# Kernel tuning notes

Hardware: AMD Instinct MI355X
Metric: run time of the kernel (lower is better)

## Reference

```python
import jax, jax.numpy as jnp
import numpy as np

# --- module hyperparameters (from init_kwargs) ---
NUM_HEADS = 16
ATTN_DIM = 1024
HEAD_DIM = ATTN_DIM // NUM_HEADS  # 64
NUM_RF = 256                      # FAVOR random features per head
CONV_CH = 1024
GROUPS = 4
M_SCALE = 256                     # num_features_per_scale
GAMMAS = (0.5, 1.0, 2.0)          # gamma_list
NY_LANDMARKS = 64                 # == HEAD_DIM so shapes compose
NY_GAMMA = 1.0
EPS = 1e-6


def setup_inputs() -> dict:
    key = jax.random.key(0)
    ks = jax.random.split(key, 12)
    B, S, C = 2, 4096, CONV_CH
    G, Ms = len(GAMMAS), M_SCALE
    x = jax.random.normal(ks[0], (B, S, C), dtype=jnp.float32)
    # grouped Conv1D kernels (WIO layout): [ksize, Cin/groups, Cout], one per q/k/v
    conv_k = jax.random.normal(ks[1], (3, 3, C // GROUPS, C), jnp.float32) / np.sqrt(3 * (C // GROUPS))
    conv_b = jnp.zeros((3, C), jnp.float32)
    # multi-scale random-Fourier-feature weights per projection and per gamma scale
    rff_w = jax.random.normal(ks[2], (3, G, C, Ms), jnp.float32)
    rff_b = jax.random.uniform(ks[3], (3, G, Ms), jnp.float32) * (2.0 * np.pi)
    proj_w = jax.random.normal(ks[4], (3, G * Ms, ATTN_DIM), jnp.float32) / np.sqrt(G * Ms)
    proj_b = jnp.zeros((3, ATTN_DIM), jnp.float32)
    # FAVOR+ projection matrix (shared across heads) and Nystrom landmarks
    omega = jax.random.normal(ks[5], (HEAD_DIM, NUM_RF), jnp.float32)
    landmarks = jax.random.normal(ks[6], (NY_LANDMARKS, HEAD_DIM), jnp.float32)
    out_w = jax.random.normal(ks[7], (ATTN_DIM, ATTN_DIM), jnp.float32) / np.sqrt(ATTN_DIM)
    out_b = jnp.zeros((ATTN_DIM,), jnp.float32)
    return {"x": x, "conv_k": conv_k, "conv_b": conv_b, "rff_w": rff_w, "rff_b": rff_b,
            "proj_w": proj_w, "proj_b": proj_b, "omega": omega, "landmarks": landmarks,
            "out_w": out_w, "out_b": out_b}


def _rotary(seq_len, dh, dtype):
    inv = 1.0 / (10000.0 ** (jnp.arange(0, dh, 2, dtype=jnp.float32) / dh))
    f = jnp.arange(seq_len, dtype=jnp.float32)[:, None] * inv[None, :]  # [S, dh/2]
    emb = jnp.concatenate([f, f], axis=-1)  # [S, dh]
    return jnp.sin(emb).astype(dtype), jnp.cos(emb).astype(dtype)


def _apply_rope(x, sin, cos):
    # x: [B,H,S,D]; rotate-half RoPE
    d = x.shape[-1] // 2
    rot = jnp.concatenate([-x[..., d:], x[..., :d]], axis=-1)
    return x * cos + rot * sin


def _projection(x, ck, cb, rw, rb, pw, pb):
    # ProjectionWithKernel: grouped conv -> multi-scale RFF kernel map -> dense
    h = jax.lax.conv_general_dilated(x, ck, (1,), 'SAME',
                                     dimension_numbers=('NWC', 'WIO', 'NWC'),
                                     feature_group_count=GROUPS) + cb
    g = jnp.sqrt(2.0 * jnp.array(GAMMAS, dtype=x.dtype))[:, None]  # [G,1]
    z = jnp.cos(jnp.einsum('bsc,gcm->bsgm', h, rw) * g + rb)       # [B,S,G,Ms]
    feats = (z * jnp.sqrt(2.0 / M_SCALE)).reshape(x.shape[0], x.shape[1], -1)
    return feats @ pw + pb  # [B,S,ATTN_DIM]


def _favor(x, omega):
    # FAVOR+ positive random features: exp(x.w - |x|^2/2) / sqrt(m)
    norm = 0.5 * jnp.sum(x * x, axis=-1, keepdims=True)
    return jnp.exp(jnp.einsum('bhsd,dm->bhsm', x, omega) - norm) / jnp.sqrt(float(omega.shape[-1]))


def _nystrom(k, landmarks):
    # RBF features against landmarks (normalized by dim to keep exp in range)
    d = k.shape[-1]
    d2 = (jnp.sum(k * k, -1, keepdims=True) + jnp.sum(landmarks * landmarks, -1)
          - 2.0 * jnp.einsum('bhsd,ld->bhsl', k, landmarks))
    return jnp.exp(-NY_GAMMA * d2 / d)  # [B,H,S,L], L == HEAD_DIM


def reference(x, conv_k, conv_b, rff_w, rff_b, proj_w, proj_b, omega, landmarks, out_w, out_b):
    B, S, _ = x.shape
    qkv = [_projection(x, conv_k[i], conv_b[i], rff_w[i], rff_b[i], proj_w[i], proj_b[i])
           for i in range(3)]
    split = lambda t: t.reshape(B, S, NUM_HEADS, HEAD_DIM).transpose(0, 2, 1, 3)
    q, k, v = map(split, qkv)  # [B,H,S,Dh]
    sin, cos = _rotary(S, HEAD_DIM, x.dtype)
    q = _apply_rope(q, sin, cos)
    k = _apply_rope(k, sin, cos)
    k = _nystrom(k, landmarks)               # [B,H,S,Dh]
    qp = _favor(q, omega)                    # [B,H,S,M]
    kp = _favor(k, omega)                    # [B,H,S,M]
    denom = jnp.einsum('bhse,bhe->bhs', qp, jnp.sum(kp, axis=2))[..., None]
    kv = jnp.einsum('bhse,bhsd->bhed', kp, v)          # [B,H,M,Dh]
    num = jnp.einsum('bhse,bhed->bhsd', qp, kv)        # [B,H,S,Dh]
    out = num / (denom + EPS)
    out = out.transpose(0, 2, 1, 3).reshape(B, S, ATTN_DIM)
    return out @ out_w + out_b  # dropout is identity at inference
```

## Files before the change

### kernel.cpp

```cpp
#include <hip/hip_runtime.h>
#include <math.h>


using f32x4 = __attribute__((ext_vector_type(4))) float;
using s16x8 = __attribute__((ext_vector_type(8))) short;

__device__ __forceinline__ unsigned short f2bf(float x) {
  unsigned u = __float_as_uint(x);
  unsigned r = u + 0x7fffu + ((u >> 16) & 1u);
  return (unsigned short)(r >> 16);
}
__device__ __forceinline__ float bf2f(unsigned short h) {
  return __uint_as_float(((unsigned)h) << 16);
}

__device__ __forceinline__ void gload16(const void* g, void* l) {
  __builtin_amdgcn_global_load_lds(
      (const __attribute__((address_space(1))) void*)g,
      (__attribute__((address_space(3))) void*)l, 16, 0, 0);
}

__global__ __launch_bounds__(256) void split_prep_kernel(
    const float* __restrict__ in, unsigned short* __restrict__ ohi,
    unsigned short* __restrict__ olo, int n8)
{
  const int i = blockIdx.x * 256 + threadIdx.x;
  if (i >= n8) return;
  const float4 f0 = ((const float4*)in)[i * 2];
  const float4 f1 = ((const float4*)in)[i * 2 + 1];
  const float v[8] = {f0.x, f0.y, f0.z, f0.w, f1.x, f1.y, f1.z, f1.w};
  s16x8 hi, lo;
  #pragma unroll
  for (int u = 0; u < 8; ++u) {
    const unsigned short hh = f2bf(v[u]);
    hi[u] = (short)hh;
    lo[u] = (short)f2bf(v[u] - bf2f(hh));
  }
  ((s16x8*)ohi)[i] = hi;
  ((s16x8*)olo)[i] = lo;
}

template<int WM>
__global__ __launch_bounds__(256) void wconv_kernel(
    const float* __restrict__ in0, unsigned short* __restrict__ ohi,
    unsigned short* __restrict__ olo)
{
  int K, N;
  const float* in;
  unsigned short *oh, *ol = nullptr;
  const int z = blockIdx.z;
  if constexpr (WM == 0) {
    K = 768; N = 1024;
    in = in0 + (size_t)z * 786432;
    oh = ohi + (size_t)z * 786432; ol = olo + (size_t)z * 786432;
  } else if constexpr (WM == 1) {
    K = 1024; N = 256;
    const int i = z / 3, g = z % 3;
    in = in0 + (size_t)i * 786432 + (size_t)g * 262144;
    oh = ohi + (size_t)i * 786432 + (size_t)g * 262144;
    ol = olo + (size_t)i * 786432 + (size_t)g * 262144;
  } else if constexpr (WM == 2) {
    K = 768; N = 1024;
    in = in0 + (size_t)z * 786432; oh = ohi + (size_t)z * 786432;
  } else {
    K = 1024; N = 1024; in = in0; oh = ohi;
  }
  const int k0 = blockIdx.x * 64, n0 = blockIdx.y * 64;
  __shared__ float t[64][65];
  const int tid = threadIdx.x, tn = tid & 63, tr = tid >> 6;
  #pragma unroll 4
  for (int p = 0; p < 16; ++p) {
    const int kk = p * 4 + tr;
    t[kk][tn] = in[(size_t)(k0 + kk) * N + n0 + tn];
  }
  __syncthreads();
  #pragma unroll 4
  for (int p = 0; p < 16; ++p) {
    const int nn = p * 4 + tr;
    const float v = t[tn][nn];
    const unsigned short hi = f2bf(v);
    oh[(size_t)(n0 + nn) * K + k0 + tn] = hi;
    if constexpr (WM <= 1)
      ol[(size_t)(n0 + nn) * K + k0 + tn] = f2bf(v - bf2f(hi));
  }
}

__global__ __launch_bounds__(256) void omega_prep_kernel(
    const float* __restrict__ omega, unsigned short* __restrict__ oThi,
    unsigned short* __restrict__ oTlo)
{
  const int idx = blockIdx.x * 256 + threadIdx.x;
  const int m = idx >> 6, d = idx & 63;
  const float v = omega[d * 256 + m];
  const unsigned short hi = f2bf(v);
  oThi[idx] = hi;
  oTlo[idx] = f2bf(v - bf2f(hi));
}

__global__ __launch_bounds__(256) void vt_kernel(
    const float* __restrict__ V, unsigned short* __restrict__ VT)
{
  const int bh = blockIdx.x, sb = blockIdx.y;
  const int b = bh >> 4, h = bh & 15;
  __shared__ float t[64][65];
  const int tid = threadIdx.x, tn = tid & 63, tr = tid >> 6;
  #pragma unroll 4
  for (int p = 0; p < 16; ++p)
    t[p * 4 + tr][tn] =
        V[(size_t)(b * 4096 + sb * 64 + p * 4 + tr) * 1024 + h * 64 + tn];
  __syncthreads();
  #pragma unroll 4
  for (int p = 0; p < 16; ++p)
    VT[((size_t)bh * 80 + p * 4 + tr) * 4096 + sb * 64 + tn] =
        f2bf(t[tn][p * 4 + tr]);
  #pragma unroll
  for (int p = 0; p < 4; ++p) {
    const int rr = p * 4 + tr;
    VT[((size_t)bh * 80 + 64 + rr) * 4096 + sb * 64 + tn] =
        (rr == 0) ? 0x3F80 : 0;
  }
}

template<int MODE>
__global__ __launch_bounds__(256, MODE >= 2 ? 4 : 3) void gemm_mfma(
    const unsigned short* __restrict__ Ahi, const unsigned short* __restrict__ Alo,
    const unsigned short* __restrict__ Bhig, const unsigned short* __restrict__ Blog,
    const float* __restrict__ bias, const float2* __restrict__ tab,
    float* __restrict__ Cf, unsigned short* __restrict__ C1,
    unsigned short* __restrict__ C2,
    int M, int N, int K)
{
  constexpr bool SPLIT = (MODE <= 1);
  __shared__ alignas(16) char smem[SPLIT ? 32768 : 16384];
  char* const sAhi = smem;
  char* const sBhi = smem + (SPLIT ? 16384 : 8192);
  char* const sAlo = smem + 8192;
  char* const sBlo = smem + 24576;

  const int gx = gridDim.x, gy = gridDim.y;
  const int L = blockIdx.x + gx * (blockIdx.y + gy * blockIdx.z);
  const int nwg = gx * gy * gridDim.z;
  const int logical = (L & 7) * (nwg >> 3) + (L >> 3);
  const int bx = logical % gx;
  const int by = (logical / gx) % gy;
  const int z = logical / (gx * gy);

  if constexpr (MODE == 0) {
    Bhig += (size_t)z * 786432; Blog += (size_t)z * 786432;
    bias += z * 1024;
    C1 += (size_t)z * 8388608; C2 += (size_t)z * 8388608;
  } else if constexpr (MODE == 1) {
    Ahi += (size_t)z * 8388608; Alo += (size_t)z * 8388608;
    Bhig += (size_t)z * 786432; Blog += (size_t)z * 786432;
    bias += z * 768;
    C1 += (size_t)z * 6291456;
  } else if constexpr (MODE == 2) {
    Ahi += (size_t)z * 6291456;
    Bhig += (size_t)z * 786432;
    bias += z * 1024;
    Cf += (size_t)z * 8388608;
  }

  const int tid = threadIdx.x;
  const int n0 = bx * 128;
  const int m0 = by * 128;

  const int lane = tid & 63, wid = tid >> 6;
  const int wr = wid >> 1, wc = wid & 1;
  const int fr = lane & 15, kc = lane >> 4;
  const int fsw = ((fr >> 1) & 3) << 4;

  const int seg0 = wid * 2;
  const int r0 = seg0 * 16 + (lane >> 2);
  const int r1 = r0 + 16;
  const int cp = lane & 3;
  const int c0e = (cp ^ ((r0 >> 1) & 3)) * 8;
  const int c1e = (cp ^ ((r1 >> 1) & 3)) * 8;
  char* const dA0 = sAhi + seg0 * 1024;  char* const dA1 = dA0 + 1024;
  char* const dL0 = sAlo + seg0 * 1024;  char* const dL1 = dL0 + 1024;
  char* const dB0 = sBhi + seg0 * 1024;  char* const dB1 = dB0 + 1024;
  char* const dBl0 = sBlo + seg0 * 1024; char* const dBl1 = dBl0 + 1024;

  f32x4 acc[4][4];
  #pragma unroll
  for (int i = 0; i < 4; ++i)
    #pragma unroll
    for (int j = 0; j < 4; ++j) acc[i][j] = f32x4{0.f, 0.f, 0.f, 0.f};

  for (int k0 = 0; k0 < K; k0 += 32) {
    __syncthreads();
    if constexpr (MODE == 0) {
      const int t = k0 >> 8;
      const int cb = (n0 >> 8) * 256 + (k0 & 255);
      const int g0 = m0 + r0, g1 = m0 + r1;
      int s0 = (g0 & 4095) + t - 1; s0 = s0 < 0 ? 0 : (s0 > 4095 ? 4095 : s0);
      int s1 = (g1 & 4095) + t - 1; s1 = s1 < 0 ? 0 : (s1 > 4095 ? 4095 : s1);
      const size_t o0 = ((size_t)((g0 >> 12) * 4096 + s0)) * 1024 + cb;
      const size_t o1 = ((size_t)((g1 >> 12) * 4096 + s1)) * 1024 + cb;
      gload16(Ahi + o0 + c0e, dA0);
      gload16(Ahi + o1 + c1e, dA1);
      gload16(Alo + o0 + c0e, dL0);
      gload16(Alo + o1 + c1e, dL1);
    } else {
      const size_t o0 = (size_t)(m0 + r0) * K + k0;
      const size_t o1 = (size_t)(m0 + r1) * K + k0;
      gload16(Ahi + o0 + c0e, dA0);
      gload16(Ahi + o1 + c1e, dA1);
      if constexpr (SPLIT) {
        gload16(Alo + o0 + c0e, dL0);
        gload16(Alo + o1 + c1e, dL1);
      }
    }
    {
      const size_t o0 = (size_t)(n0 + r0) * K + k0;
      const size_t o1 = (size_t)(n0 + r1) * K + k0;
      gload16(Bhig + o0 + c0e, dB0);
      gload16(Bhig + o1 + c1e, dB1);
      if constexpr (SPLIT) {
        gload16(Blog + o0 + c0e, dBl0);
        gload16(Blog + o1 + c1e, dBl1);
      }
    }
    __syncthreads();

    if constexpr (MODE == 0) {
      const int t = k0 >> 8;
      int zr = -1;
      if (t == 0 && (m0 & 4095) == 0) zr = 0;
      if (t == 2 && (m0 & 4095) == 3968) zr = 127;
      if (zr >= 0) {
        if (tid < 8) {
          char* buf = (tid < 4) ? sAhi : sAlo;
          *(s16x8*)(buf + zr * 64 + (tid & 3) * 16) = s16x8{0,0,0,0,0,0,0,0};
        }
        __syncthreads();
      }
    }

    s16x8 Af[4], Al[4], Bf[4], Bl[4];
    #pragma unroll
    for (int i = 0; i < 4; ++i) {
      const int off = (wr * 64 + i * 16 + fr) * 64 + ((kc * 16) ^ fsw);
      Af[i] = *(const s16x8*)(sAhi + off);
      if constexpr (SPLIT) Al[i] = *(const s16x8*)(sAlo + off);
    }
    #pragma unroll
    for (int j = 0; j < 4; ++j) {
      const int off = (wc * 64 + j * 16 + fr) * 64 + ((kc * 16) ^ fsw);
      Bf[j] = *(const s16x8*)(sBhi + off);
      if constexpr (SPLIT) Bl[j] = *(const s16x8*)(sBlo + off);
    }
    #pragma unroll
    for (int i = 0; i < 4; ++i)
      #pragma unroll
      for (int j = 0; j < 4; ++j) {
        acc[i][j] = __builtin_amdgcn_mfma_f32_16x16x32_bf16(Af[i], Bf[j], acc[i][j], 0, 0, 0);
        if constexpr (SPLIT) {
          acc[i][j] = __builtin_amdgcn_mfma_f32_16x16x32_bf16(Af[i], Bl[j], acc[i][j], 0, 0, 0);
          acc[i][j] = __builtin_amdgcn_mfma_f32_16x16x32_bf16(Al[i], Bf[j], acc[i][j], 0, 0, 0);
        }
      }
  }

  if constexpr (MODE == 2) {
    #pragma unroll
    for (int i = 0; i < 4; ++i)
      #pragma unroll
      for (int j2 = 0; j2 < 2; ++j2) {
        const int col0 = n0 + wc * 64 + j2 * 16 + fr;
        const int jr = col0 & 31;
        const float b0 = bias[col0], b1 = bias[col0 + 32];
        #pragma unroll
        for (int rr = 0; rr < 4; ++rr) {
          const int row = m0 + wr * 64 + i * 16 + kc * 4 + rr;
          float v0 = acc[i][j2][rr] + b0;
          float v1 = acc[i][j2 + 2][rr] + b1;
          if (z < 2) {
            const float2 cs = tab[((row & 4095) << 5) | jr];
            const float rr0 = v0 * cs.x - v1 * cs.y;
            const float rr1 = v1 * cs.x + v0 * cs.y;
            v0 = rr0; v1 = rr1;
          }
          Cf[(size_t)row * N + col0] = v0;
          Cf[(size_t)row * N + col0 + 32] = v1;
        }
      }
  } else {
    #pragma unroll
    for (int i = 0; i < 4; ++i)
      #pragma unroll
      for (int j = 0; j < 4; ++j) {
        const int col = n0 + wc * 64 + j * 16 + fr;
        #pragma unroll
        for (int rr = 0; rr < 4; ++rr) {
          const int row = m0 + wr * 64 + i * 16 + kc * 4 + rr;
          const float v = acc[i][j][rr];
          if constexpr (MODE == 0) {
            const float hv = v + bias[col];
            const unsigned short hh = f2bf(hv);
            C1[(size_t)row * N + col] = hh;
            C2[(size_t)row * N + col] = f2bf(hv - bf2f(hh));
          } else if constexpr (MODE == 1) {
            const int g = col >> 8;
            const float sg = (g == 0) ? 1.0f : ((g == 1) ? 1.41421356237309515f : 2.0f);
            const float zc = cosf(v * sg + bias[col]) * 0.08838834764831845f;
            C1[(size_t)row * N + col] = f2bf(zc);
          } else {
            Cf[(size_t)row * N + col] = v + bias[col];
          }
        }
      }
  }
}

__global__ __launch_bounds__(256) void rope_table_kernel(float2* __restrict__ tab)
{
  const int idx = blockIdx.x * 256 + threadIdx.x;
  const int j = idx & 31, s = idx >> 5;
  const double inv = pow(10000.0, -(double)j * (1.0 / 32.0));
  double sd, cd;
  sincos((double)s * inv, &sd, &cd);
  tab[idx] = make_float2((float)cd, (float)sd);
}

__global__ __launch_bounds__(256) void nystrom_kernel(
    const float* __restrict__ Kb, const float* __restrict__ lm,
    float* __restrict__ kny)
{
  __shared__ float lmT[64][65];
  __shared__ float lnorm[64];
  const int tid = threadIdx.x;
  for (int idx = tid; idx < 4096; idx += 256)
    lmT[idx & 63][idx >> 6] = lm[idx];
  if (tid < 64) {
    float s = 0.f;
    #pragma unroll
    for (int d = 0; d < 64; ++d) { const float v = lm[tid * 64 + d]; s = fmaf(v, v, s); }
    lnorm[tid] = s;
  }
  __syncthreads();
  const int lane = tid & 63;
  const int nw = gridDim.x * 4;
  for (int row = blockIdx.x * 4 + (tid >> 6); row < 131072; row += nw) {
    const float kd = Kb[(size_t)row * 64 + lane];
    float nk = kd * kd;
    #pragma unroll
    for (int o = 32; o > 0; o >>= 1) nk += __shfl_xor(nk, o, 64);
    float dot = 0.f;
    #pragma unroll
    for (int d = 0; d < 64; ++d) dot = fmaf(__shfl(kd, d, 64), lmT[d][lane], dot);
    kny[(size_t)row * 64 + lane] = __expf((2.f * dot - nk - lnorm[lane]) * 0.015625f);
  }
}

__global__ __launch_bounds__(512) void favor_k_mfma(
    const float* __restrict__ kny,
    const unsigned short* __restrict__ oThi, const unsigned short* __restrict__ oTlo,
    const unsigned short* __restrict__ VT, float* __restrict__ KVp)
{
  const int bid = blockIdx.x;
  const int bh = bid >> 3, chunk = bid & 7;
  const int b = bh >> 4, h = bh & 15;
  const int s0 = chunk * 512;
  const int tid = threadIdx.x, lane = tid & 63, wid = tid >> 6;
  const int fr = lane & 15, kc = lane >> 4;
  const int m0w = wid * 32;

  __shared__ unsigned short P[256][40];
  __shared__ float T[8][32][84];

  s16x8 whi[2][2], wlo[2][2];
  #pragma unroll
  for (int c = 0; c < 2; ++c)
    #pragma unroll
    for (int ks = 0; ks < 2; ++ks) {
      const size_t off = (size_t)(m0w + c * 16 + fr) * 64 + ks * 32 + kc * 8;
      whi[c][ks] = *(const s16x8*)(oThi + off);
      wlo[c][ks] = *(const s16x8*)(oTlo + off);
    }

  f32x4 acc2[2][5];
  #pragma unroll
  for (int i = 0; i < 2; ++i)
    #pragma unroll
    for (int j = 0; j < 5; ++j) acc2[i][j] = f32x4{0.f, 0.f, 0.f, 0.f};

  for (int st = 0; st < 512; st += 32) {
    s16x8 ahi[2][2], alo[2][2];
    float nrm[2];
    #pragma unroll
    for (int r = 0; r < 2; ++r) {
      float part = 0.f;
      #pragma unroll
      for (int ks = 0; ks < 2; ++ks) {
        const float* ap = kny +
            ((size_t)((b * 4096 + s0 + st + r * 16 + fr) * 16 + h)) * 64 + ks * 32 + kc * 8;
        const float4 f0 = ((const float4*)ap)[0];
        const float4 f1 = ((const float4*)ap)[1];
        float v[8] = {f0.x, f0.y, f0.z, f0.w, f1.x, f1.y, f1.z, f1.w};
        #pragma unroll
        for (int u = 0; u < 8; ++u) {
          part = fmaf(v[u], v[u], part);
          const unsigned short hh = f2bf(v[u]);
          ahi[r][ks][u] = (short)hh;
          alo[r][ks][u] = (short)f2bf(v[u] - bf2f(hh));
        }
      }
      part += __shfl_xor(part, 16);
      part += __shfl_xor(part, 32);
      nrm[r] = 0.5f * part;
    }
    __syncthreads();
    #pragma unroll
    for (int r = 0; r < 2; ++r)
      #pragma unroll
      for (int c = 0; c < 2; ++c) {
        f32x4 s1 = f32x4{0.f, 0.f, 0.f, 0.f};
        #pragma unroll
        for (int ks = 0; ks < 2; ++ks) {
          s1 = __builtin_amdgcn_mfma_f32_16x16x32_bf16(alo[r][ks], whi[c][ks], s1, 0, 0, 0);
          s1 = __builtin_amdgcn_mfma_f32_16x16x32_bf16(ahi[r][ks], wlo[c][ks], s1, 0, 0, 0);
          s1 = __builtin_amdgcn_mfma_f32_16x16x32_bf16(ahi[r][ks], whi[c][ks], s1, 0, 0, 0);
        }
        #pragma unroll
        for (int reg = 0; reg < 4; ++reg) {
          const int sl = kc * 4 + reg;
          const float nn = __shfl(nrm[r], sl);
          const float p = __expf(s1[reg] - nn - 2.772588722239781f);
          P[m0w + c * 16 + fr][r * 16 + sl] = f2bf(p);
        }
      }
    __syncthreads();
    s16x8 b2[5];
    #pragma unroll
    for (int nf = 0; nf < 5; ++nf)
      b2[nf] = *(const s16x8*)(VT + ((size_t)bh * 80 + nf * 16 + fr) * 4096 +
                               s0 + st + kc * 8);
    #pragma unroll
    for (int mf = 0; mf < 2; ++mf) {
      const s16x8 a2 = *(const s16x8*)&P[m0w + mf * 16 + fr][kc * 8];
      #pragma unroll
      for (int nf = 0; nf < 5; ++nf)
        acc2[mf][nf] = __builtin_amdgcn_mfma_f32_16x16x32_bf16(a2, b2[nf], acc2[mf][nf], 0, 0, 0);
    }
  }
  #pragma unroll
  for (int mf = 0; mf < 2; ++mf)
    #pragma unroll
    for (int nf = 0; nf < 5; ++nf)
      #pragma unroll
      for (int reg = 0; reg < 4; ++reg)
        T[wid][mf * 16 + kc * 4 + reg][nf * 16 + fr] = acc2[mf][nf][reg];
  __syncthreads();
  #pragma unroll
  for (int i = 0; i < 40; ++i) {
    const int flat = i * 64 + lane;
    const int n = flat >> 5, ml = flat & 31;
    KVp[((size_t)bid * 80 + n) * 256 + m0w + ml] = T[wid][ml][n];
  }
}

__global__ __launch_bounds__(256) void reduce_kvxt_kernel(
    const float* __restrict__ KVp, unsigned short* __restrict__ KVXT)
{
  const int bh = blockIdx.x;
  const int m = threadIdx.x;
  for (int n = 0; n < 80; ++n) {
    float s = 0.f;
    #pragma unroll
    for (int c = 0; c < 8; ++c)
      s += KVp[((size_t)(bh * 8 + c) * 80 + n) * 256 + m];
    KVXT[((size_t)bh * 80 + n) * 256 + m] = f2bf(s);
  }
}

__global__ __launch_bounds__(512) void favor_q_mfma(
    const float* __restrict__ Q,
    const unsigned short* __restrict__ oThi, const unsigned short* __restrict__ oTlo,
    const unsigned short* __restrict__ KVXT, unsigned short* __restrict__ O)
{
  const int bid = blockIdx.x;
  const int bh = bid >> 4, chunk = bid & 15;
  const int b = bh >> 4, h = bh & 15;
  const int s0 = chunk * 256;
  const int tid = threadIdx.x, lane = tid & 63, wid = tid >> 6;
  const int fr = lane & 15, kc = lane >> 4;
  const int ws0 = s0 + wid * 32;

  __shared__ unsigned short KX[80][264];
  __shared__ unsigned short P[8][32][66];

  for (int i = tid; i < 80 * 256; i += 512)
    KX[i >> 8][i & 255] = KVXT[(size_t)bh * 80 * 256 + i];
  __syncthreads();

  s16x8 ahi[2][2], alo[2][2];
  float nrm[2];
  #pragma unroll
  for (int r = 0; r < 2; ++r) {
    float part = 0.f;
    #pragma unroll
    for (int ks = 0; ks < 2; ++ks) {
      const float* ap = Q + ((size_t)(b * 4096 + ws0 + r * 16 + fr)) * 1024 +
                        h * 64 + ks * 32 + kc * 8;
      const float4 f0 = ((const float4*)ap)[0];
      const float4 f1 = ((const float4*)ap)[1];
      float v[8] = {f0.x, f0.y, f0.z, f0.w, f1.x, f1.y, f1.z, f1.w};
      #pragma unroll
      for (int u = 0; u < 8; ++u) {
        part = fmaf(v[u], v[u], part);
        const unsigned short hh = f2bf(v[u]);
        ahi[r][ks][u] = (short)hh;
        alo[r][ks][u] = (short)f2bf(v[u] - bf2f(hh));
      }
    }
    part += __shfl_xor(part, 16);
    part += __shfl_xor(part, 32);
    nrm[r] = 0.5f * part;
  }

  f32x4 acc2[2][5];
  #pragma unroll
  for (int i = 0; i < 2; ++i)
    #pragma unroll
    for (int j = 0; j < 5; ++j) acc2[i][j] = f32x4{0.f, 0.f, 0.f, 0.f};

  for (int mc = 0; mc < 4; ++mc) {
    __syncthreads();
    #pragma unroll
    for (int r = 0; r < 2; ++r)
      #pragma unroll
      for (int c = 0; c < 4; ++c) {
        f32x4 s1 = f32x4{0.f, 0.f, 0.f, 0.f};
        #pragma unroll
        for (int ks = 0; ks < 2; ++ks) {
          const size_t off = (size_t)(mc * 64 + c * 16 + fr) * 64 + ks * 32 + kc * 8;
          const s16x8 bh1 = *(const s16x8*)(oThi + off);
          const s16x8 bl1 = *(const s16x8*)(oTlo + off);
          s1 = __builtin_amdgcn_mfma_f32_16x16x32_bf16(alo[r][ks], bh1, s1, 0, 0, 0);
          s1 = __builtin_amdgcn_mfma_f32_16x16x32_bf16(ahi[r][ks], bl1, s1, 0, 0, 0);
          s1 = __builtin_amdgcn_mfma_f32_16x16x32_bf16(ahi[r][ks], bh1, s1, 0, 0, 0);
        }
        #pragma unroll
        for (int reg = 0; reg < 4; ++reg) {
          const int sl = kc * 4 + reg;
          const float nn = __shfl(nrm[r], sl);
          const float p = __expf(s1[reg] - nn - 2.772588722239781f);
          P[wid][r * 16 + sl][c * 16 + fr] = f2bf(p);
        }
      }
    __syncthreads();
    #pragma unroll
    for (int ks2 = 0; ks2 < 2; ++ks2) {
      s16x8 b2[5];
      #pragma unroll
      for (int nf = 0; nf < 5; ++nf)
        b2[nf] = *(const s16x8*)&KX[nf * 16 + fr][mc * 64 + ks2 * 32 + kc * 8];
      #pragma unroll
      for (int r = 0; r < 2; ++r) {
        const s16x8 a2 = *(const s16x8*)&P[wid][r * 16 + fr][ks2 * 32 + kc * 8];
        #pragma unroll
        for (int nf = 0; nf < 5; ++nf)
          acc2[r][nf] = __builtin_amdgcn_mfma_f32_16x16x32_bf16(a2, b2[nf], acc2[r][nf], 0, 0, 0);
      }
    }
  }
  #pragma unroll
  for (int r = 0; r < 2; ++r)
    #pragma unroll
    for (int reg = 0; reg < 4; ++reg) {
      const int s = ws0 + r * 16 + kc * 4 + reg;
      const float dv = __shfl(acc2[r][4][reg], lane & 48) + 1e-6f;
      #pragma unroll
      for (int nf = 0; nf < 4; ++nf)
        O[(size_t)(b * 4096 + s) * 1024 + h * 64 + nf * 16 + fr] =
            f2bf(acc2[r][nf][reg] / dv);
    }
}

extern "C" void kernel_launch(void* const* d_in, const int* in_sizes, int n_in,
                              void* d_out, int out_size, void* d_ws, size_t ws_size,
                              hipStream_t stream)
{
  const float* x      = (const float*)d_in[0];
  const float* conv_k = (const float*)d_in[1];
  const float* conv_b = (const float*)d_in[2];
  const float* rff_w  = (const float*)d_in[3];
  const float* rff_b  = (const float*)d_in[4];
  const float* proj_w = (const float*)d_in[5];
  const float* proj_b = (const float*)d_in[6];
  const float* omega  = (const float*)d_in[7];
  const float* lm     = (const float*)d_in[8];
  const float* out_w  = (const float*)d_in[9];
  const float* out_b  = (const float*)d_in[10];

  char* wsb = (char*)d_ws;
  size_t o = 0;
  auto alloc = [&](size_t bytes) {
    char* p = wsb + o;
    o = (o + bytes + 255) & ~(size_t)255;
    return p;
  };
  unsigned short* Wc_hi = (unsigned short*)alloc(4718592);
  unsigned short* Wc_lo = (unsigned short*)alloc(4718592);
  unsigned short* Wr_hi = (unsigned short*)alloc(4718592);
  unsigned short* Wr_lo = (unsigned short*)alloc(4718592);
  unsigned short* Wp    = (unsigned short*)alloc(4718592);
  unsigned short* Wo    = (unsigned short*)alloc(2097152);
  unsigned short* oThi  = (unsigned short*)alloc(32768);
  unsigned short* oTlo  = (unsigned short*)alloc(32768);
  float2* tab           = (float2*)alloc(1048576);
  char* RB = alloc(41943040);
  unsigned short* xhi   = (unsigned short*)RB;
  unsigned short* xlo   = (unsigned short*)(RB + 16777216);
  unsigned short* feats = (unsigned short*)RB;
  unsigned short* VT    = (unsigned short*)RB;
  unsigned short* Obf   = (unsigned short*)(RB + 20971520);
  unsigned short* KVXT  = (unsigned short*)(RB + 37748736);
  char* RC = alloc(100663296);
  unsigned short* hhi   = (unsigned short*)RC;
  unsigned short* hlo   = (unsigned short*)(RC + 50331648);
  float* QKV            = (float*)RC;
  float* kny = (float*)alloc(33554432);
  float* KVp = (float*)alloc(20971520);

  dim3 blk(256);
  split_prep_kernel<<<4096, blk, 0, stream>>>(x, xhi, xlo, 1048576);
  wconv_kernel<0><<<dim3(12, 16, 3), blk, 0, stream>>>(conv_k, Wc_hi, Wc_lo);
  wconv_kernel<1><<<dim3(16, 4, 9),  blk, 0, stream>>>(rff_w, Wr_hi, Wr_lo);
  wconv_kernel<2><<<dim3(12, 16, 3), blk, 0, stream>>>(proj_w, Wp, nullptr);
  wconv_kernel<3><<<dim3(16, 16, 1), blk, 0, stream>>>(out_w, Wo, nullptr);
  omega_prep_kernel<<<64, blk, 0, stream>>>(omega, oThi, oTlo);
  rope_table_kernel<<<512, blk, 0, stream>>>(tab);

  gemm_mfma<0><<<dim3(8, 64, 3), blk, 0, stream>>>(
      xhi, xlo, Wc_hi, Wc_lo, conv_b, nullptr,
      nullptr, hhi, hlo, 8192, 1024, 768);
  gemm_mfma<1><<<dim3(6, 64, 3), blk, 0, stream>>>(
      hhi, hlo, Wr_hi, Wr_lo, rff_b, nullptr,
      nullptr, feats, nullptr, 8192, 768, 1024);
  gemm_mfma<2><<<dim3(8, 64, 3), blk, 0, stream>>>(
      feats, nullptr, Wp, nullptr, proj_b, tab,
      QKV, nullptr, nullptr, 8192, 1024, 768);

  float* Qb = QKV;
  float* Kb = QKV + 8388608;
  float* Vb = QKV + 16777216;
  vt_kernel<<<dim3(32, 64), blk, 0, stream>>>(Vb, VT);
  nystrom_kernel<<<512, blk, 0, stream>>>(Kb, lm, kny);
  favor_k_mfma<<<256, dim3(512), 0, stream>>>(kny, oThi, oTlo, VT, KVp);
  reduce_kvxt_kernel<<<32, blk, 0, stream>>>(KVp, KVXT);
  favor_q_mfma<<<512, dim3(512), 0, stream>>>(Qb, oThi, oTlo, KVXT, Obf);
  gemm_mfma<3><<<dim3(8, 64), blk, 0, stream>>>(
      Obf, nullptr, Wo, nullptr, out_b, nullptr,
      (float*)d_out, nullptr, nullptr, 8192, 1024, 1024);
}
```

Baseline: 1.058 ms.

## Drop bf16 hi/lo split in FAVOR stages and move Nystrom onto MFMA

Removes the three-term hi/lo bf16 emulation in favor_k and favor_q, using a single bf16 MFMA against bf16 omega. Rewrites the Nystrom kernel to use MFMA. It now writes bf16 kernel features plus precomputed half squared norms, which favor_k reads directly instead of recomputing. It also raises gemm_mfma launch bounds to 4 waves for the split modes. The aim is to cut MFMA count, memory traffic and conversion work, at the cost of lower precision in the feature maps and possibly more register pressure in the split GEMMs.

```diff
diff --git a/kernel.cpp b/kernel.cpp
--- a/kernel.cpp
+++ b/kernel.cpp
@@ -86,15 +86,11 @@
 }
 
 __global__ __launch_bounds__(256) void omega_prep_kernel(
-    const float* __restrict__ omega, unsigned short* __restrict__ oThi,
-    unsigned short* __restrict__ oTlo)
+    const float* __restrict__ omega, unsigned short* __restrict__ oThi)
 {
   const int idx = blockIdx.x * 256 + threadIdx.x;
   const int m = idx >> 6, d = idx & 63;
-  const float v = omega[d * 256 + m];
-  const unsigned short hi = f2bf(v);
-  oThi[idx] = hi;
-  oTlo[idx] = f2bf(v - bf2f(hi));
+  oThi[idx] = f2bf(omega[d * 256 + m]);
 }
 
 __global__ __launch_bounds__(256) void vt_kernel(
@@ -122,7 +118,7 @@
 }
 
 template<int MODE>
-__global__ __launch_bounds__(256, MODE >= 2 ? 4 : 3) void gemm_mfma(
+__global__ __launch_bounds__(256, 4) void gemm_mfma(
     const unsigned short* __restrict__ Ahi, const unsigned short* __restrict__ Alo,
     const unsigned short* __restrict__ Bhig, const unsigned short* __restrict__ Blog,
     const float* __restrict__ bias, const float2* __restrict__ tab,
@@ -323,15 +319,18 @@
   tab[idx] = make_float2((float)cd, (float)sd);
 }
 
-__global__ __launch_bounds__(256) void nystrom_kernel(
+__global__ __launch_bounds__(256) void nystrom_mfma(
     const float* __restrict__ Kb, const float* __restrict__ lm,
-    float* __restrict__ kny)
-{
-  __shared__ float lmT[64][65];
+    unsigned short* __restrict__ kny, float* __restrict__ knorm)
+{
+  const int bid = blockIdx.x;
+  const int bh = bid >> 4, chunk = bid & 15;
+  const int b = bh >> 4, h = bh & 15;
+  const int tid = threadIdx.x, lane = tid & 63, wid = tid >> 6;
+  const int fr = lane & 15, kc = lane >> 4;
+  const int ws0 = chunk * 256 + wid * 64;
+
   __shared__ float lnorm[64];
-  const int tid = threadIdx.x;
-  for (int idx = tid; idx < 4096; idx += 256)
-    lmT[idx & 63][idx >> 6] = lm[idx];
   if (tid < 64) {
     float s = 0.f;
     #pragma unroll
@@ -339,23 +338,69 @@
     lnorm[tid] = s;
   }
   __syncthreads();
-  const int lane = tid & 63;
-  const int nw = gridDim.x * 4;
-  for (int row = blockIdx.x * 4 + (tid >> 6); row < 131072; row += nw) {
-    const float kd = Kb[(size_t)row * 64 + lane];
-    float nk = kd * kd;
-    #pragma unroll
-    for (int o = 32; o > 0; o >>= 1) nk += __shfl_xor(nk, o, 64);
-    float dot = 0.f;
-    #pragma unroll
-    for (int d = 0; d < 64; ++d) dot = fmaf(__shfl(kd, d, 64), lmT[d][lane], dot);
-    kny[(size_t)row * 64 + lane] = __expf((2.f * dot - nk - lnorm[lane]) * 0.015625f);
+
+  s16x8 bfr[4][2];
+  #pragma unroll
+  for (int c = 0; c < 4; ++c)
+    #pragma unroll
+    for (int ks = 0; ks < 2; ++ks) {
+      const float* lp = lm + (c * 16 + fr) * 64 + ks * 32 + kc * 8;
+      #pragma unroll
+      for (int u = 0; u < 8; ++u) bfr[c][ks][u] = (short)f2bf(lp[u]);
+    }
+
+  #pragma unroll
+  for (int r = 0; r < 4; ++r) {
+    const int s_r = ws0 + r * 16 + fr;
+    const float* ap = Kb + ((size_t)(b * 4096 + s_r)) * 1024 + h * 64;
+    s16x8 afr[2];
+    float part = 0.f;
+    #pragma unroll
+    for (int ks = 0; ks < 2; ++ks) {
+      const float4 f0 = *(const float4*)(ap + ks * 32 + kc * 8);
+      const float4 f1 = *(const float4*)(ap + ks * 32 + kc * 8 + 4);
+      const float v[8] = {f0.x, f0.y, f0.z, f0.w, f1.x, f1.y, f1.z, f1.w};
+      #pragma unroll
+      for (int u = 0; u < 8; ++u) {
+        part = fmaf(v[u], v[u], part);
+        afr[ks][u] = (short)f2bf(v[u]);
+      }
+    }
+    part += __shfl_xor(part, 16);
+    part += __shfl_xor(part, 32);
+
+    float sq[4] = {0.f, 0.f, 0.f, 0.f};
+    #pragma unroll
+    for (int c = 0; c < 4; ++c) {
+      f32x4 acc = f32x4{0.f, 0.f, 0.f, 0.f};
+      acc = __builtin_amdgcn_mfma_f32_16x16x32_bf16(afr[0], bfr[c][0], acc, 0, 0, 0);
+      acc = __builtin_amdgcn_mfma_f32_16x16x32_bf16(afr[1], bfr[c][1], acc, 0, 0, 0);
+      const float ln = lnorm[c * 16 + fr];
+      #pragma unroll
+      for (int reg = 0; reg < 4; ++reg) {
+        const float nk = __shfl(part, kc * 4 + reg);
+        const float val = __expf((2.f * acc[reg] - nk - ln) * 0.015625f);
+        sq[reg] = fmaf(val, val, sq[reg]);
+        const int srow = ws0 + r * 16 + kc * 4 + reg;
+        kny[((size_t)(b * 4096 + srow) * 16 + h) * 64 + c * 16 + fr] = f2bf(val);
+      }
+    }
+    #pragma unroll
+    for (int reg = 0; reg < 4; ++reg) {
+      float s2 = sq[reg];
+      s2 += __shfl_xor(s2, 1); s2 += __shfl_xor(s2, 2);
+      s2 += __shfl_xor(s2, 4); s2 += __shfl_xor(s2, 8);
+      if (fr == 0) {
+        const int srow = ws0 + r * 16 + kc * 4 + reg;
+        knorm[(size_t)(b * 4096 + srow) * 16 + h] = 0.5f * s2;
+      }
+    }
   }
 }
 
 __global__ __launch_bounds__(512) void favor_k_mfma(
-    const float* __restrict__ kny,
-    const unsigned short* __restrict__ oThi, const unsigned short* __restrict__ oTlo,
+    const unsigned short* __restrict__ kny, const float* __restrict__ knorm,
+    const unsigned short* __restrict__ oThi,
     const unsigned short* __restrict__ VT, float* __restrict__ KVp)
 {
   const int bid = blockIdx.x;
@@ -369,15 +414,12 @@
   __shared__ unsigned short P[256][40];
   __shared__ float T[8][32][84];
 
-  s16x8 whi[2][2], wlo[2][2];
+  s16x8 whi[2][2];
   #pragma unroll
   for (int c = 0; c < 2; ++c)
     #pragma unroll
-    for (int ks = 0; ks < 2; ++ks) {
-      const size_t off = (size_t)(m0w + c * 16 + fr) * 64 + ks * 32 + kc * 8;
-      whi[c][ks] = *(const s16x8*)(oThi + off);
-      wlo[c][ks] = *(const s16x8*)(oTlo + off);
-    }
+    for (int ks = 0; ks < 2; ++ks)
+      whi[c][ks] = *(const s16x8*)(oThi + (size_t)(m0w + c * 16 + fr) * 64 + ks * 32 + kc * 8);
 
   f32x4 acc2[2][5];
   #pragma unroll
@@ -386,29 +428,14 @@
     for (int j = 0; j < 5; ++j) acc2[i][j] = f32x4{0.f, 0.f, 0.f, 0.f};
 
   for (int st = 0; st < 512; st += 32) {
-    s16x8 ahi[2][2], alo[2][2];
+    s16x8 a1[2][2];
     float nrm[2];
     #pragma unroll
     for (int r = 0; r < 2; ++r) {
-      float part = 0.f;
-      #pragma unroll
-      for (int ks = 0; ks < 2; ++ks) {
-        const float* ap = kny +
-            ((size_t)((b * 4096 + s0 + st + r * 16 + fr) * 16 + h)) * 64 + ks * 32 + kc * 8;
-        const float4 f0 = ((const float4*)ap)[0];
-        const float4 f1 = ((const float4*)ap)[1];
-        float v[8] = {f0.x, f0.y, f0.z, f0.w, f1.x, f1.y, f1.z, f1.w};
-        #pragma unroll
-        for (int u = 0; u < 8; ++u) {
-          part = fmaf(v[u], v[u], part);
-          const unsigned short hh = f2bf(v[u]);
-          ahi[r][ks][u] = (short)hh;
-          alo[r][ks][u] = (short)f2bf(v[u] - bf2f(hh));
-        }
-      }
-      part += __shfl_xor(part, 16);
-      part += __shfl_xor(part, 32);
-      nrm[r] = 0.5f * part;
+      const size_t kidx = (size_t)(b * 4096 + s0 + st + r * 16 + fr) * 16 + h;
+      a1[r][0] = *(const s16x8*)(kny + kidx * 64 + kc * 8);
+      a1[r][1] = *(const s16x8*)(kny + kidx * 64 + 32 + kc * 8);
+      nrm[r] = knorm[kidx];
     }
     __syncthreads();
     #pragma unroll
@@ -416,12 +443,8 @@
       #pragma unroll
       for (int c = 0; c < 2; ++c) {
         f32x4 s1 = f32x4{0.f, 0.f, 0.f, 0.f};
-        #pragma unroll
-        for (int ks = 0; ks < 2; ++ks) {
-          s1 = __builtin_amdgcn_mfma_f32_16x16x32_bf16(alo[r][ks], whi[c][ks], s1, 0, 0, 0);
-          s1 = __builtin_amdgcn_mfma_f32_16x16x32_bf16(ahi[r][ks], wlo[c][ks], s1, 0, 0, 0);
-          s1 = __builtin_amdgcn_mfma_f32_16x16x32_bf16(ahi[r][ks], whi[c][ks], s1, 0, 0, 0);
-        }
+        s1 = __builtin_amdgcn_mfma_f32_16x16x32_bf16(a1[r][0], whi[c][0], s1, 0, 0, 0);
+        s1 = __builtin_amdgcn_mfma_f32_16x16x32_bf16(a1[r][1], whi[c][1], s1, 0, 0, 0);
         #pragma unroll
         for (int reg = 0; reg < 4; ++reg) {
           const int sl = kc * 4 + reg;
@@ -475,8 +498,7 @@
 }
 
 __global__ __launch_bounds__(512) void favor_q_mfma(
-    const float* __restrict__ Q,
-    const unsigned short* __restrict__ oThi, const unsigned short* __restrict__ oTlo,
+    const float* __restrict__ Q, const unsigned short* __restrict__ oThi,
     const unsigned short* __restrict__ KVXT, unsigned short* __restrict__ O)
 {
   const int bid = blockIdx.x;
@@ -494,7 +516,7 @@
     KX[i >> 8][i & 255] = KVXT[(size_t)bh * 80 * 256 + i];
   __syncthreads();
 
-  s16x8 ahi[2][2], alo[2][2];
+  s16x8 ahi[2][2];
   float nrm[2];
   #pragma unroll
   for (int r = 0; r < 2; ++r) {
@@ -505,13 +527,11 @@
                         h * 64 + ks * 32 + kc * 8;
       const float4 f0 = ((const float4*)ap)[0];
       const float4 f1 = ((const float4*)ap)[1];
-      float v[8] = {f0.x, f0.y, f0.z, f0.w, f1.x, f1.y, f1.z, f1.w};
+      const float v[8] = {f0.x, f0.y, f0.z, f0.w, f1.x, f1.y, f1.z, f1.w};
       #pragma unroll
       for (int u = 0; u < 8; ++u) {
         part = fmaf(v[u], v[u], part);
-        const unsigned short hh = f2bf(v[u]);
-        ahi[r][ks][u] = (short)hh;
-        alo[r][ks][u] = (short)f2bf(v[u] - bf2f(hh));
+        ahi[r][ks][u] = (short)f2bf(v[u]);
       }
     }
     part += __shfl_xor(part, 16);
@@ -536,9 +556,6 @@
         for (int ks = 0; ks < 2; ++ks) {
           const size_t off = (size_t)(mc * 64 + c * 16 + fr) * 64 + ks * 32 + kc * 8;
           const s16x8 bh1 = *(const s16x8*)(oThi + off);
-          const s16x8 bl1 = *(const s16x8*)(oTlo + off);
-          s1 = __builtin_amdgcn_mfma_f32_16x16x32_bf16(alo[r][ks], bh1, s1, 0, 0, 0);
-          s1 = __builtin_amdgcn_mfma_f32_16x16x32_bf16(ahi[r][ks], bl1, s1, 0, 0, 0);
           s1 = __builtin_amdgcn_mfma_f32_16x16x32_bf16(ahi[r][ks], bh1, s1, 0, 0, 0);
         }
         #pragma unroll
@@ -621,8 +638,11 @@
   unsigned short* hhi   = (unsigned short*)RC;
   unsigned short* hlo   = (unsigned short*)(RC + 50331648);
   float* QKV            = (float*)RC;
-  float* kny = (float*)alloc(33554432);
+  char* RE = alloc(33554432);
+  unsigned short* knyb  = (unsigned short*)RE;
+  float* knorm          = (float*)(RE + 16777216);
   float* KVp = (float*)alloc(20971520);
+  (void)oTlo; (void)ws_size;
 
   dim3 blk(256);
   split_prep_kernel<<<4096, blk, 0, stream>>>(x, xhi, xlo, 1048576);
@@ -630,7 +650,7 @@
   wconv_kernel<1><<<dim3(16, 4, 9),  blk, 0, stream>>>(rff_w, Wr_hi, Wr_lo);
   wconv_kernel<2><<<dim3(12, 16, 3), blk, 0, stream>>>(proj_w, Wp, nullptr);
   wconv_kernel<3><<<dim3(16, 16, 1), blk, 0, stream>>>(out_w, Wo, nullptr);
-  omega_prep_kernel<<<64, blk, 0, stream>>>(omega, oThi, oTlo);
+  omega_prep_kernel<<<64, blk, 0, stream>>>(omega, oThi);
   rope_table_kernel<<<512, blk, 0, stream>>>(tab);
 
   gemm_mfma<0><<<dim3(8, 64, 3), blk, 0, stream>>>(
@@ -647,10 +667,10 @@
   float* Kb = QKV + 8388608;
   float* Vb = QKV + 16777216;
   vt_kernel<<<dim3(32, 64), blk, 0, stream>>>(Vb, VT);
-  nystrom_kernel<<<512, blk, 0, stream>>>(Kb, lm, kny);
-  favor_k_mfma<<<256, dim3(512), 0, stream>>>(kny, oThi, oTlo, VT, KVp);
+  nystrom_mfma<<<512, blk, 0, stream>>>(Kb, lm, knyb, knorm);
+  favor_k_mfma<<<256, dim3(512), 0, stream>>>(knyb, knorm, oThi, VT, KVp);
   reduce_kvxt_kernel<<<32, blk, 0, stream>>>(KVp, KVXT);
-  favor_q_mfma<<<512, dim3(512), 0, stream>>>(Qb, oThi, oTlo, KVXT, Obf);
+  favor_q_mfma<<<512, dim3(512), 0, stream>>>(Qb, oThi, KVXT, Obf);
   gemm_mfma<3><<<dim3(8, 64), blk, 0, stream>>>(
       Obf, nullptr, Wo, nullptr, out_b, nullptr,
       (float*)d_out, nullptr, nullptr, 8192, 1024, 1024);
```

Result: faster. 925.3 us (-12.5%).
